# Optimization experiments

Measured on AMD Instinct MI355X. Metric: run time of the kernel, lower is better.

The kernel has to match this reference:

```python
import jax, jax.numpy as jnp
import numpy as np

N = 8192       # nodes
E = 262144     # edges (avg degree 32)
F_IN, H, L = 512, 256, 64


def setup_inputs() -> dict:
    key = jax.random.key(0)
    ks = jax.random.split(key, 8)
    features = jax.random.normal(ks[0], (N, F_IN), dtype=jnp.float32)
    src = jax.random.randint(ks[1], (E,), 0, N)
    dst = jax.random.randint(ks[2], (E,), 0, N)
    # nn.Linear weights are [out_feats, in_feats]; scale ~ kaiming-ish small init
    W1 = jax.random.normal(ks[3], (H, F_IN), dtype=jnp.float32) * (1.0 / np.sqrt(F_IN))
    b1 = jnp.zeros((H,), dtype=jnp.float32)
    W2 = jax.random.normal(ks[4], (L, H), dtype=jnp.float32) * (1.0 / np.sqrt(H))
    b2 = jnp.zeros((L,), dtype=jnp.float32)
    W3 = jax.random.normal(ks[5], (L, H), dtype=jnp.float32) * (1.0 / np.sqrt(H))
    b3 = jnp.zeros((L,), dtype=jnp.float32)
    return {"features": features, "src": src, "dst": dst,
            "W1": W1, "b1": b1, "W2": W2, "b2": b2, "W3": W3, "b3": b3}


def _gcn_agg(h, src, dst):
    # DGL copy_src + sum: gather source node features along edges, scatter-sum to dst
    return jax.ops.segment_sum(h[src], dst, num_segments=N)  # [N, d]


def reference(features, src, dst, W1, b1, W2, b2, W3, b3):
    # GCN layer 1: aggregate then linear + relu  (dropout=0 -> identity)
    agg1 = _gcn_agg(features, src, dst)                 # [N, F_IN]
    hidden = jax.nn.relu(agg1 @ W1.T + b1)              # [N, H]
    # GCN layers 2 & 3 share the aggregated hidden (linear activation)
    agg2 = _gcn_agg(hidden, src, dst)                   # [N, H]
    mu = agg2 @ W2.T + b2                               # [N, L]
    logvar = agg2 @ W3.T + b3                           # [N, L]
    # eval-mode reparameterize: z = mu
    z = mu
    # inner-product decoder with sigmoid
    adj = jax.nn.sigmoid(z @ z.T)                       # [N, N]
    return adj, mu, logvar
```

## Files before the change

kernel.cpp:

```cpp
#include <hip/hip_runtime.h>
#include <hip/hip_bf16.h>

#define N_NODES 8192
#define N_EDGES 262144

typedef __attribute__((ext_vector_type(8))) short short8v;
typedef __attribute__((ext_vector_type(4))) float float4v;

static __device__ __forceinline__ unsigned short f2bf(float f) {
    unsigned u = __float_as_uint(f);
    unsigned r = (u + 0x7FFF + ((u >> 16) & 1)) >> 16;
    return (unsigned short)r;
}
static __device__ __forceinline__ float bf2f(unsigned short h) {
    return __uint_as_float(((unsigned)h) << 16);
}


__global__ __launch_bounds__(256) void hist_kernel(const int* __restrict__ dst, int* __restrict__ deg) {
    int e = blockIdx.x * 256 + threadIdx.x;
    if (e < N_EDGES) atomicAdd(&deg[dst[e]], 1);
}

__global__ __launch_bounds__(1024) void scan_kernel(const int* __restrict__ deg, int* __restrict__ offs) {
    __shared__ int sums[1024];
    int t = threadIdx.x;
    int v[8];
    int s = 0;
#pragma unroll
    for (int i = 0; i < 8; i++) { v[i] = deg[t * 8 + i]; s += v[i]; }
    sums[t] = s;
    __syncthreads();
    for (int off = 1; off < 1024; off <<= 1) {
        int x = (t >= off) ? sums[t - off] : 0;
        __syncthreads();
        sums[t] += x;
        __syncthreads();
    }
    int ex = (t == 0) ? 0 : sums[t - 1];
#pragma unroll
    for (int i = 0; i < 8; i++) { offs[t * 8 + i] = ex; ex += v[i]; }
    if (t == 1023) offs[N_NODES] = ex;
}

__global__ __launch_bounds__(256) void scatter_kernel(const int* __restrict__ src, const int* __restrict__ dst,
                                                      const int* __restrict__ offs, int* __restrict__ cur,
                                                      int* __restrict__ csr) {
    int e = blockIdx.x * 256 + threadIdx.x;
    if (e < N_EDGES) {
        int d = dst[e];
        int p = atomicAdd(&cur[d], 1);
        csr[offs[d] + p] = src[e];
    }
}


__global__ __launch_bounds__(256) void prep_cast_kernel(const float* __restrict__ X, const float* __restrict__ W1,
                                                        const float* __restrict__ W2, const float* __restrict__ W3,
                                                        unsigned short* __restrict__ Xb,
                                                        unsigned short* __restrict__ W1b,
                                                        unsigned short* __restrict__ W23b) {
    int i4 = (blockIdx.x * 256 + threadIdx.x) * 4;
    const float* srcp;
    unsigned short* dstp;
    int off;
    if (i4 < 4194304)      { srcp = X;  dstp = Xb;           off = i4; }
    else if (i4 < 4325376) { srcp = W1; dstp = W1b;          off = i4 - 4194304; }
    else if (i4 < 4341760) { srcp = W2; dstp = W23b;         off = i4 - 4325376; }
    else                   { srcp = W3; dstp = W23b + 16384; off = i4 - 4341760; }
    float4 v = *(const float4*)&srcp[off];
    ushort4 o = {f2bf(v.x), f2bf(v.y), f2bf(v.z), f2bf(v.w)};
    *(ushort4*)&dstp[off] = o;
}


template <int MI, int NJ, int WN>
__global__ __launch_bounds__(256) void gemm_nt_mfma(const unsigned short* __restrict__ A,
                                                    const unsigned short* __restrict__ B,
                                                    unsigned short* __restrict__ C,
                                                    int N, int K) {
    constexpr int MW = 4 / WN;
    const int tid = threadIdx.x;
    const int lane = tid & 63;
    const int w = tid >> 6;
    const int r = lane & 15, q = lane >> 4;
    const int m0 = blockIdx.x * (MI * 16 * MW) + (w / WN) * (MI * 16);
    const int n0 = blockIdx.y * (NJ * 16 * WN) + (w % WN) * (NJ * 16);
    float4v acc[MI][NJ] = {};
    for (int k = 0; k < K; k += 32) {
        short8v a[MI], b[NJ];
#pragma unroll
        for (int i = 0; i < MI; i++)
            a[i] = *(const short8v*)&A[(size_t)(m0 + i * 16 + r) * K + k + q * 8];
#pragma unroll
        for (int j = 0; j < NJ; j++)
            b[j] = *(const short8v*)&B[(size_t)(n0 + j * 16 + r) * K + k + q * 8];
#pragma unroll
        for (int i = 0; i < MI; i++)
#pragma unroll
            for (int j = 0; j < NJ; j++)
                acc[i][j] = __builtin_amdgcn_mfma_f32_16x16x32_bf16(a[i], b[j], acc[i][j], 0, 0, 0);
    }
#pragma unroll
    for (int i = 0; i < MI; i++)
#pragma unroll
        for (int j = 0; j < NJ; j++) {
            int col = n0 + j * 16 + r;
#pragma unroll
            for (int t = 0; t < 4; t++) {
                int row = m0 + i * 16 + q * 4 + t;
                C[(size_t)row * N + col] = f2bf(acc[i][j][t]);
            }
        }
}


__global__ __launch_bounds__(256) void agg_relu_kernel(const unsigned short* __restrict__ Yb,
                                                       const int* __restrict__ offs,
                                                       const int* __restrict__ csr, const float* __restrict__ bias,
                                                       unsigned short* __restrict__ out) {
    int node = blockIdx.x * 4 + (threadIdx.x >> 6);
    int lane = threadIdx.x & 63;
    int s = offs[node], e = offs[node + 1];
    float4 acc = {0.f, 0.f, 0.f, 0.f};
    int i = s;
    for (; i + 1 < e; i += 2) {
        int u0 = csr[i], u1 = csr[i + 1];
        ushort4 v0 = *(const ushort4*)&Yb[(size_t)u0 * 256 + lane * 4];
        ushort4 v1 = *(const ushort4*)&Yb[(size_t)u1 * 256 + lane * 4];
        acc.x += bf2f(v0.x) + bf2f(v1.x);
        acc.y += bf2f(v0.y) + bf2f(v1.y);
        acc.z += bf2f(v0.z) + bf2f(v1.z);
        acc.w += bf2f(v0.w) + bf2f(v1.w);
    }
    if (i < e) {
        int u = csr[i];
        ushort4 v = *(const ushort4*)&Yb[(size_t)u * 256 + lane * 4];
        acc.x += bf2f(v.x); acc.y += bf2f(v.y); acc.z += bf2f(v.z); acc.w += bf2f(v.w);
    }
    float4 b = *(const float4*)&bias[lane * 4];
    ushort4 o;
    o.x = f2bf(fmaxf(acc.x + b.x, 0.f));
    o.y = f2bf(fmaxf(acc.y + b.y, 0.f));
    o.z = f2bf(fmaxf(acc.z + b.z, 0.f));
    o.w = f2bf(fmaxf(acc.w + b.w, 0.f));
    *(ushort4*)&out[(size_t)node * 256 + lane * 4] = o;
}


__global__ __launch_bounds__(256) void agg_split_kernel(const unsigned short* __restrict__ Zb,
                                                        const int* __restrict__ offs,
                                                        const int* __restrict__ csr, const float* __restrict__ b2,
                                                        const float* __restrict__ b3, float* __restrict__ mu,
                                                        float* __restrict__ lv, unsigned short* __restrict__ zb) {
    int node = blockIdx.x * 4 + (threadIdx.x >> 6);
    int lane = threadIdx.x & 63;
    int s = offs[node], e = offs[node + 1];
    float2 acc = {0.f, 0.f};
    int i = s;
    for (; i + 1 < e; i += 2) {
        int u0 = csr[i], u1 = csr[i + 1];
        ushort2 v0 = *(const ushort2*)&Zb[(size_t)u0 * 128 + lane * 2];
        ushort2 v1 = *(const ushort2*)&Zb[(size_t)u1 * 128 + lane * 2];
        acc.x += bf2f(v0.x) + bf2f(v1.x);
        acc.y += bf2f(v0.y) + bf2f(v1.y);
    }
    if (i < e) {
        int u = csr[i];
        ushort2 v = *(const ushort2*)&Zb[(size_t)u * 128 + lane * 2];
        acc.x += bf2f(v.x); acc.y += bf2f(v.y);
    }
    int col = lane * 2;
    if (col < 64) {
        acc.x += b2[col]; acc.y += b2[col + 1];
        *(float2*)&mu[(size_t)node * 64 + col] = acc;
        ushort2 q = {f2bf(acc.x), f2bf(acc.y)};
        *(ushort2*)&zb[(size_t)node * 64 + col] = q;
    } else {
        col -= 64;
        acc.x += b3[col]; acc.y += b3[col + 1];
        *(float2*)&lv[(size_t)node * 64 + col] = acc;
    }
}


__global__ __launch_bounds__(256) void adj_mfma_kernel(const unsigned short* __restrict__ zb,
                                                       float* __restrict__ out) {
    const int tid = threadIdx.x;
    const int lane = tid & 63;
    const int wid = tid >> 6;
    const int waveM = wid >> 1, waveN = wid & 1;
    const int m_base = blockIdx.x * 128 + waveM * 64;
    const int n_base = blockIdx.y * 128 + waveN * 64;
    const int r = lane & 15;
    const int q = lane >> 4;

    short8v a[4][2], b[4][2];
#pragma unroll
    for (int i = 0; i < 4; i++)
#pragma unroll
        for (int s = 0; s < 2; s++) {
            a[i][s] = *(const short8v*)&zb[(size_t)(m_base + i * 16 + r) * 64 + s * 32 + q * 8];
            b[i][s] = *(const short8v*)&zb[(size_t)(n_base + i * 16 + r) * 64 + s * 32 + q * 8];
        }

    float4v acc[4][4] = {};
#pragma unroll
    for (int s = 0; s < 2; s++)
#pragma unroll
        for (int i = 0; i < 4; i++)
#pragma unroll
            for (int j = 0; j < 4; j++)
                acc[i][j] = __builtin_amdgcn_mfma_f32_16x16x32_bf16(a[i][s], b[j][s], acc[i][j], 0, 0, 0);

#pragma unroll
    for (int i = 0; i < 4; i++)
#pragma unroll
        for (int j = 0; j < 4; j++) {
            int col = n_base + j * 16 + r;
#pragma unroll
            for (int t = 0; t < 4; t++) {
                int row = m_base + i * 16 + q * 4 + t;
                float v = 1.0f / (1.0f + __expf(-acc[i][j][t]));
                out[(size_t)row * N_NODES + col] = v;
            }
        }
}


extern "C" void kernel_launch(void* const* d_in, const int* in_sizes, int n_in,
                              void* d_out, int out_size, void* d_ws, size_t ws_size,
                              hipStream_t stream) {
    const float* X   = (const float*)d_in[0];
    const int*   src = (const int*)d_in[1];
    const int*   dst = (const int*)d_in[2];
    const float* W1  = (const float*)d_in[3];
    const float* b1  = (const float*)d_in[4];
    const float* W2  = (const float*)d_in[5];
    const float* b2  = (const float*)d_in[6];
    const float* W3  = (const float*)d_in[7];
    const float* b3  = (const float*)d_in[8];

    float* out    = (float*)d_out;
    float* adj    = out;
    float* mu_out = out + (size_t)N_NODES * N_NODES;
    float* lv_out = mu_out + (size_t)N_NODES * 64;

    char* ws = (char*)d_ws;
    size_t off = 0;
    auto alloc = [&](size_t bytes) -> void* {
        void* p = ws + off;
        off += (bytes + 1023) & ~(size_t)1023;
        return p;
    };
    int* deg            = (int*)alloc(N_NODES * 4);
    int* cur            = (int*)alloc(N_NODES * 4);
    int* offs           = (int*)alloc((N_NODES + 1) * 4);
    int* csr            = (int*)alloc(N_EDGES * 4);
    unsigned short* Xb  = (unsigned short*)alloc((size_t)N_NODES * 512 * 2);
    unsigned short* W1b = (unsigned short*)alloc(256 * 512 * 2);
    unsigned short* W23b= (unsigned short*)alloc(128 * 256 * 2);
    unsigned short* Y1b = (unsigned short*)alloc((size_t)N_NODES * 256 * 2);
    unsigned short* Hb  = (unsigned short*)alloc((size_t)N_NODES * 256 * 2);
    unsigned short* Zb  = (unsigned short*)alloc((size_t)N_NODES * 128 * 2);
    unsigned short* zb  = (unsigned short*)alloc((size_t)N_NODES * 64 * 2);

    hipMemsetAsync(deg, 0, 2 * N_NODES * sizeof(int), stream);
    hist_kernel<<<N_EDGES / 256, 256, 0, stream>>>(dst, deg);
    scan_kernel<<<1, 1024, 0, stream>>>(deg, offs);
    scatter_kernel<<<N_EDGES / 256, 256, 0, stream>>>(src, dst, offs, cur, csr);
    prep_cast_kernel<<<4256, 256, 0, stream>>>(X, W1, W2, W3, Xb, W1b, W23b);

    gemm_nt_mfma<4, 2, 4><<<dim3(128, 2), 256, 0, stream>>>(Xb, W1b, Y1b, 256, 512);
    agg_relu_kernel<<<N_NODES / 4, 256, 0, stream>>>(Y1b, offs, csr, b1, Hb);
    gemm_nt_mfma<4, 1, 4><<<dim3(128, 2), 256, 0, stream>>>(Hb, W23b, Zb, 128, 256);
    agg_split_kernel<<<N_NODES / 4, 256, 0, stream>>>(Zb, offs, csr, b2, b3, mu_out, lv_out, zb);
    adj_mfma_kernel<<<dim3(64, 64), 256, 0, stream>>>(zb, adj);
}
```

Baseline: 383.5 us.

## Fuse histogram with cast, seed cursors in scan, unroll gathers, nontemporal adj stores

Merges the degree histogram into the cast kernel as extra blocks, and has the scan write absolute cursor offsets so the scatter no longer reads offs. The neighbour-aggregation loops are unrolled to four edges with two accumulators for more memory-level parallelism. The GEMM launches use smaller M tiles with twice as many blocks, and the 256MB adjacency output uses nontemporal stores to avoid cache pollution. Together these cut launches and per-kernel latency, but change summation order slightly.

Result: slower. 419.2 us (+9.3%).

```diff
diff --git a/kernel.cpp b/kernel.cpp
--- a/kernel.cpp
+++ b/kernel.cpp
@@ -17,50 +17,19 @@
 }
 
 
-__global__ __launch_bounds__(256) void hist_kernel(const int* __restrict__ dst, int* __restrict__ deg) {
-    int e = blockIdx.x * 256 + threadIdx.x;
-    if (e < N_EDGES) atomicAdd(&deg[dst[e]], 1);
-}
-
-__global__ __launch_bounds__(1024) void scan_kernel(const int* __restrict__ deg, int* __restrict__ offs) {
-    __shared__ int sums[1024];
-    int t = threadIdx.x;
-    int v[8];
-    int s = 0;
-#pragma unroll
-    for (int i = 0; i < 8; i++) { v[i] = deg[t * 8 + i]; s += v[i]; }
-    sums[t] = s;
-    __syncthreads();
-    for (int off = 1; off < 1024; off <<= 1) {
-        int x = (t >= off) ? sums[t - off] : 0;
-        __syncthreads();
-        sums[t] += x;
-        __syncthreads();
-    }
-    int ex = (t == 0) ? 0 : sums[t - 1];
-#pragma unroll
-    for (int i = 0; i < 8; i++) { offs[t * 8 + i] = ex; ex += v[i]; }
-    if (t == 1023) offs[N_NODES] = ex;
-}
-
-__global__ __launch_bounds__(256) void scatter_kernel(const int* __restrict__ src, const int* __restrict__ dst,
-                                                      const int* __restrict__ offs, int* __restrict__ cur,
-                                                      int* __restrict__ csr) {
-    int e = blockIdx.x * 256 + threadIdx.x;
-    if (e < N_EDGES) {
-        int d = dst[e];
-        int p = atomicAdd(&cur[d], 1);
-        csr[offs[d] + p] = src[e];
-    }
-}
-
-
-__global__ __launch_bounds__(256) void prep_cast_kernel(const float* __restrict__ X, const float* __restrict__ W1,
+__global__ __launch_bounds__(256) void hist_prep_kernel(const int* __restrict__ dst, int* __restrict__ deg,
+                                                        const float* __restrict__ X, const float* __restrict__ W1,
                                                         const float* __restrict__ W2, const float* __restrict__ W3,
                                                         unsigned short* __restrict__ Xb,
                                                         unsigned short* __restrict__ W1b,
                                                         unsigned short* __restrict__ W23b) {
-    int i4 = (blockIdx.x * 256 + threadIdx.x) * 4;
+    int b = blockIdx.x;
+    if (b < 1024) {
+        int e = b * 256 + threadIdx.x;
+        atomicAdd(&deg[dst[e]], 1);
+        return;
+    }
+    int i4 = ((b - 1024) * 256 + threadIdx.x) * 4;
     const float* srcp;
     unsigned short* dstp;
     int off;
@@ -71,6 +40,37 @@
     float4 v = *(const float4*)&srcp[off];
     ushort4 o = {f2bf(v.x), f2bf(v.y), f2bf(v.z), f2bf(v.w)};
     *(ushort4*)&dstp[off] = o;
+}
+
+
+__global__ __launch_bounds__(1024) void scan_kernel(const int* __restrict__ deg, int* __restrict__ offs,
+                                                    int* __restrict__ cur) {
+    __shared__ int sums[1024];
+    int t = threadIdx.x;
+    int v[8];
+    int s = 0;
+#pragma unroll
+    for (int i = 0; i < 8; i++) { v[i] = deg[t * 8 + i]; s += v[i]; }
+    sums[t] = s;
+    __syncthreads();
+    for (int off = 1; off < 1024; off <<= 1) {
+        int x = (t >= off) ? sums[t - off] : 0;
+        __syncthreads();
+        sums[t] += x;
+        __syncthreads();
+    }
+    int ex = (t == 0) ? 0 : sums[t - 1];
+#pragma unroll
+    for (int i = 0; i < 8; i++) { offs[t * 8 + i] = ex; cur[t * 8 + i] = ex; ex += v[i]; }
+    if (t == 1023) offs[N_NODES] = ex;
+}
+
+__global__ __launch_bounds__(256) void scatter_kernel(const int* __restrict__ src, const int* __restrict__ dst,
+                                                      int* __restrict__ cur, int* __restrict__ csr) {
+    int e = blockIdx.x * 256 + threadIdx.x;
+    int d = dst[e];
+    int p = atomicAdd(&cur[d], 1);
+    csr[p] = src[e];
 }
 
 
@@ -122,28 +122,30 @@
     int node = blockIdx.x * 4 + (threadIdx.x >> 6);
     int lane = threadIdx.x & 63;
     int s = offs[node], e = offs[node + 1];
-    float4 acc = {0.f, 0.f, 0.f, 0.f};
+    float4 acc0 = {0.f, 0.f, 0.f, 0.f}, acc1 = {0.f, 0.f, 0.f, 0.f};
     int i = s;
-    for (; i + 1 < e; i += 2) {
-        int u0 = csr[i], u1 = csr[i + 1];
+    for (; i + 3 < e; i += 4) {
+        int u0 = csr[i], u1 = csr[i + 1], u2 = csr[i + 2], u3 = csr[i + 3];
         ushort4 v0 = *(const ushort4*)&Yb[(size_t)u0 * 256 + lane * 4];
         ushort4 v1 = *(const ushort4*)&Yb[(size_t)u1 * 256 + lane * 4];
-        acc.x += bf2f(v0.x) + bf2f(v1.x);
-        acc.y += bf2f(v0.y) + bf2f(v1.y);
-        acc.z += bf2f(v0.z) + bf2f(v1.z);
-        acc.w += bf2f(v0.w) + bf2f(v1.w);
-    }
-    if (i < e) {
+        ushort4 v2 = *(const ushort4*)&Yb[(size_t)u2 * 256 + lane * 4];
+        ushort4 v3 = *(const ushort4*)&Yb[(size_t)u3 * 256 + lane * 4];
+        acc0.x += bf2f(v0.x) + bf2f(v1.x); acc1.x += bf2f(v2.x) + bf2f(v3.x);
+        acc0.y += bf2f(v0.y) + bf2f(v1.y); acc1.y += bf2f(v2.y) + bf2f(v3.y);
+        acc0.z += bf2f(v0.z) + bf2f(v1.z); acc1.z += bf2f(v2.z) + bf2f(v3.z);
+        acc0.w += bf2f(v0.w) + bf2f(v1.w); acc1.w += bf2f(v2.w) + bf2f(v3.w);
+    }
+    for (; i < e; i++) {
         int u = csr[i];
         ushort4 v = *(const ushort4*)&Yb[(size_t)u * 256 + lane * 4];
-        acc.x += bf2f(v.x); acc.y += bf2f(v.y); acc.z += bf2f(v.z); acc.w += bf2f(v.w);
+        acc0.x += bf2f(v.x); acc0.y += bf2f(v.y); acc0.z += bf2f(v.z); acc0.w += bf2f(v.w);
     }
     float4 b = *(const float4*)&bias[lane * 4];
     ushort4 o;
-    o.x = f2bf(fmaxf(acc.x + b.x, 0.f));
-    o.y = f2bf(fmaxf(acc.y + b.y, 0.f));
-    o.z = f2bf(fmaxf(acc.z + b.z, 0.f));
-    o.w = f2bf(fmaxf(acc.w + b.w, 0.f));
+    o.x = f2bf(fmaxf(acc0.x + acc1.x + b.x, 0.f));
+    o.y = f2bf(fmaxf(acc0.y + acc1.y + b.y, 0.f));
+    o.z = f2bf(fmaxf(acc0.z + acc1.z + b.z, 0.f));
+    o.w = f2bf(fmaxf(acc0.w + acc1.w + b.w, 0.f));
     *(ushort4*)&out[(size_t)node * 256 + lane * 4] = o;
 }
 
@@ -156,20 +158,23 @@
     int node = blockIdx.x * 4 + (threadIdx.x >> 6);
     int lane = threadIdx.x & 63;
     int s = offs[node], e = offs[node + 1];
-    float2 acc = {0.f, 0.f};
+    float2 acc0 = {0.f, 0.f}, acc1 = {0.f, 0.f};
     int i = s;
-    for (; i + 1 < e; i += 2) {
-        int u0 = csr[i], u1 = csr[i + 1];
+    for (; i + 3 < e; i += 4) {
+        int u0 = csr[i], u1 = csr[i + 1], u2 = csr[i + 2], u3 = csr[i + 3];
         ushort2 v0 = *(const ushort2*)&Zb[(size_t)u0 * 128 + lane * 2];
         ushort2 v1 = *(const ushort2*)&Zb[(size_t)u1 * 128 + lane * 2];
-        acc.x += bf2f(v0.x) + bf2f(v1.x);
-        acc.y += bf2f(v0.y) + bf2f(v1.y);
-    }
-    if (i < e) {
+        ushort2 v2 = *(const ushort2*)&Zb[(size_t)u2 * 128 + lane * 2];
+        ushort2 v3 = *(const ushort2*)&Zb[(size_t)u3 * 128 + lane * 2];
+        acc0.x += bf2f(v0.x) + bf2f(v1.x); acc1.x += bf2f(v2.x) + bf2f(v3.x);
+        acc0.y += bf2f(v0.y) + bf2f(v1.y); acc1.y += bf2f(v2.y) + bf2f(v3.y);
+    }
+    for (; i < e; i++) {
         int u = csr[i];
         ushort2 v = *(const ushort2*)&Zb[(size_t)u * 128 + lane * 2];
-        acc.x += bf2f(v.x); acc.y += bf2f(v.y);
-    }
+        acc0.x += bf2f(v.x); acc0.y += bf2f(v.y);
+    }
+    float2 acc = {acc0.x + acc1.x, acc0.y + acc1.y};
     int col = lane * 2;
     if (col < 64) {
         acc.x += b2[col]; acc.y += b2[col + 1];
@@ -222,7 +227,7 @@
             for (int t = 0; t < 4; t++) {
                 int row = m_base + i * 16 + q * 4 + t;
                 float v = 1.0f / (1.0f + __expf(-acc[i][j][t]));
-                out[(size_t)row * N_NODES + col] = v;
+                __builtin_nontemporal_store(v, &out[(size_t)row * N_NODES + col]);
             }
         }
 }
@@ -265,15 +270,14 @@
     unsigned short* Zb  = (unsigned short*)alloc((size_t)N_NODES * 128 * 2);
     unsigned short* zb  = (unsigned short*)alloc((size_t)N_NODES * 64 * 2);
 
-    hipMemsetAsync(deg, 0, 2 * N_NODES * sizeof(int), stream);
-    hist_kernel<<<N_EDGES / 256, 256, 0, stream>>>(dst, deg);
-    scan_kernel<<<1, 1024, 0, stream>>>(deg, offs);
-    scatter_kernel<<<N_EDGES / 256, 256, 0, stream>>>(src, dst, offs, cur, csr);
-    prep_cast_kernel<<<4256, 256, 0, stream>>>(X, W1, W2, W3, Xb, W1b, W23b);
-
-    gemm_nt_mfma<4, 2, 4><<<dim3(128, 2), 256, 0, stream>>>(Xb, W1b, Y1b, 256, 512);
+    hipMemsetAsync(deg, 0, N_NODES * sizeof(int), stream);
+    hist_prep_kernel<<<5280, 256, 0, stream>>>(dst, deg, X, W1, W2, W3, Xb, W1b, W23b);
+    scan_kernel<<<1, 1024, 0, stream>>>(deg, offs, cur);
+    scatter_kernel<<<N_EDGES / 256, 256, 0, stream>>>(src, dst, cur, csr);
+
+    gemm_nt_mfma<2, 2, 4><<<dim3(256, 2), 256, 0, stream>>>(Xb, W1b, Y1b, 256, 512);
     agg_relu_kernel<<<N_NODES / 4, 256, 0, stream>>>(Y1b, offs, csr, b1, Hb);
-    gemm_nt_mfma<4, 1, 4><<<dim3(128, 2), 256, 0, stream>>>(Hb, W23b, Zb, 128, 256);
+    gemm_nt_mfma<2, 1, 4><<<dim3(256, 2), 256, 0, stream>>>(Hb, W23b, Zb, 128, 256);
     agg_split_kernel<<<N_NODES / 4, 256, 0, stream>>>(Zb, offs, csr, b2, b3, mu_out, lv_out, zb);
     adj_mfma_kernel<<<dim3(64, 64), 256, 0, stream>>>(zb, adj);
 }
```
